# Kernel optimization log

Hardware: AMD Instinct MI355X
Metric: run time of the kernel (lower is better)

Reference implementation:

```python
import jax, jax.numpy as jnp
import numpy as np

M, IN, H, OUT, B = 64, 64, 256, 1, 4096


def setup_inputs() -> dict:
    key = jax.random.key(0)
    ks = jax.random.split(key, 7)
    s1 = 1.0 / np.sqrt(IN)
    s2 = 1.0 / np.sqrt(H)
    return {
        "xs": jax.random.normal(ks[0], (M, B, IN), dtype=jnp.float32),
        "W1": jax.random.uniform(ks[1], (M, IN, H), minval=-s1, maxval=s1, dtype=jnp.float32),
        "b1": jax.random.uniform(ks[2], (M, H), minval=-s1, maxval=s1, dtype=jnp.float32),
        "W2": jax.random.uniform(ks[3], (M, H, H), minval=-s2, maxval=s2, dtype=jnp.float32),
        "b2": jax.random.uniform(ks[4], (M, H), minval=-s2, maxval=s2, dtype=jnp.float32),
        "W3": jax.random.uniform(ks[5], (M, H, OUT), minval=-s2, maxval=s2, dtype=jnp.float32),
        "b3": jax.random.uniform(ks[6], (M, OUT), minval=-s2, maxval=s2, dtype=jnp.float32),
    }


def reference(xs, W1, b1, W2, b2, W3, b3):
    # Batched over models: [M, B, in] x [M, in, h] -> [M, B, h]
    h1 = jax.nn.relu(jnp.einsum("mbi,mih->mbh", xs, W1) + b1[:, None, :])
    h2 = jax.nn.relu(jnp.einsum("mbh,mhk->mbk", h1, W2) + b2[:, None, :])
    out = jnp.einsum("mbh,mho->mbo", h2, W3) + b3[:, None, :]
    return out  # [M, B, out]
```

## Files before the change

### kernel.cpp

```cpp
#include <hip/hip_runtime.h>
#include <hip/hip_bf16.h>

#define NMODELS 64
#define BBATCH  4096
#define IN_DIM  64
#define H_DIM   256

typedef __attribute__((ext_vector_type(8))) short short8;
typedef __attribute__((ext_vector_type(4))) float floatx4;
typedef __attribute__((ext_vector_type(4))) unsigned int uint4v;
typedef __attribute__((ext_vector_type(2))) unsigned int uint2v;

__device__ __forceinline__ unsigned short f2bf(float f) {
    unsigned int u = __builtin_bit_cast(unsigned int, f);
    return (unsigned short)((u + 0x8000u) >> 16);
}
__device__ __forceinline__ unsigned int pkbf(float a, float b) {
    __hip_bfloat162 h = __float22bfloat162_rn(make_float2(a, b));
    unsigned int u;
    __builtin_memcpy(&u, &h, 4);
    return u;
}

__global__ __launch_bounds__(256) void prep_weights(const float* __restrict__ W1,
                                                    const float* __restrict__ W2,
                                                    unsigned short* __restrict__ w1t,
                                                    unsigned short* __restrict__ w2t) {
    __shared__ float lds[64][65];
    const int bid = blockIdx.x;
    const float* src;
    unsigned short* dst;
    int K, N, m, kb, nb;
    if (bid < 256) {
        m = bid >> 2; kb = 0; nb = bid & 3; K = IN_DIM; N = H_DIM;
        src = W1; dst = w1t;
    } else {
        int t = bid - 256;
        m = t >> 4; kb = (t >> 2) & 3; nb = t & 3; K = H_DIM; N = H_DIM;
        src = W2; dst = w2t;
    }
    const float* s = src + ((size_t)m * K + (size_t)kb * 64) * N + nb * 64;
    const int tid = threadIdx.x;
    const int r = tid >> 4, c4 = (tid & 15) * 4;
#pragma unroll
    for (int p = 0; p < 4; ++p) {
        int row = p * 16 + r;
        float4 v = *(const float4*)(s + (size_t)row * N + c4);
        lds[row][c4] = v.x; lds[row][c4 + 1] = v.y;
        lds[row][c4 + 2] = v.z; lds[row][c4 + 3] = v.w;
    }
    __syncthreads();
    unsigned short* dbase = dst + ((size_t)m * N + (size_t)nb * 64) * K + kb * 64;
    const int j = tid & 7;
#pragma unroll
    for (int it = 0; it < 2; ++it) {
        int n = it * 32 + (tid >> 3);
        unsigned short tmp[8];
#pragma unroll
        for (int e = 0; e < 8; ++e) tmp[e] = f2bf(lds[j * 8 + e][n]);
        *(short8*)(dbase + (size_t)n * K + j * 8) = *(const short8*)tmp;
    }
}

__global__ __launch_bounds__(256, 3) void mlp_fused(
    const float* __restrict__ xs,
    const unsigned short* __restrict__ w1t,
    const float* __restrict__ b1,
    const unsigned short* __restrict__ w2t,
    const float* __restrict__ b2,
    const float* __restrict__ w3,
    const float* __restrict__ b3,
    float* __restrict__ out)
{
    __shared__ unsigned short h1s[64 * 256];
    float* red = (float*)&h1s[0];

    const int bid  = blockIdx.x;
    const int m    = bid >> 6;
    const int tile = bid & 63;
    const int tid  = threadIdx.x;
    const int w    = tid >> 6;
    const int lane = tid & 63;
    const int q    = lane >> 4;
    const int c16  = lane & 15;
    const int sw   = c16 & 7;

    floatx4 b1v = *(const floatx4*)(b1 + m * H_DIM + w * 64 + c16 * 4);
    floatx4 b2v = *(const floatx4*)(b2 + m * H_DIM + w * 64 + c16 * 4);
    floatx4 w3v = *(const floatx4*)(w3 + m * H_DIM + w * 64 + c16 * 4);
    const float b3v = b3[m];

    const float* xrow0 = xs + ((size_t)m * BBATCH + (size_t)tile * 64) * IN_DIM;
    const unsigned short* w1p = w1t + (size_t)m * (H_DIM * IN_DIM)
                                + (w * 64 + c16 * 4) * IN_DIM + q * 8;
    const unsigned short* w2p = w2t + (size_t)m * (H_DIM * H_DIM)
                                + (w * 64 + c16 * 4) * H_DIM + q * 8;

    short8 ax[4][2];
#pragma unroll
    for (int rb = 0; rb < 4; ++rb)
#pragma unroll
        for (int kb = 0; kb < 2; ++kb) {
            const float* xp = xrow0 + (rb * 16 + c16) * IN_DIM + kb * 32 + q * 8;
            float4 v0 = *(const float4*)xp;
            float4 v1 = *(const float4*)(xp + 4);
            uint4v u;
            u[0] = pkbf(v0.x, v0.y); u[1] = pkbf(v0.z, v0.w);
            u[2] = pkbf(v1.x, v1.y); u[3] = pkbf(v1.z, v1.w);
            ax[rb][kb] = __builtin_bit_cast(short8, u);
        }

    floatx4 acc[4][4];
#pragma unroll
    for (int rb = 0; rb < 4; ++rb)
#pragma unroll
        for (int nb = 0; nb < 4; ++nb)
            acc[rb][nb] = (floatx4){0.f, 0.f, 0.f, 0.f};

    {
        short8 bw[2][4];
#pragma unroll
        for (int kb = 0; kb < 2; ++kb)
#pragma unroll
            for (int nb = 0; nb < 4; ++nb)
                bw[kb][nb] = *(const short8*)(w1p + nb * IN_DIM + kb * 32);
#pragma unroll
        for (int kb = 0; kb < 2; ++kb)
#pragma unroll
            for (int nb = 0; nb < 4; ++nb)
#pragma unroll
                for (int rb = 0; rb < 4; ++rb)
                    acc[rb][nb] = __builtin_amdgcn_mfma_f32_16x16x32_bf16(
                        ax[rb][kb], bw[kb][nb], acc[rb][nb], 0, 0, 0);
    }

    short8 bv[2][4];
#pragma unroll
    for (int nb = 0; nb < 4; ++nb)
        bv[0][nb] = *(const short8*)(w2p + nb * H_DIM);

    {
#pragma unroll
        for (int rb = 0; rb < 4; ++rb)
#pragma unroll
            for (int r = 0; r < 4; ++r) {
                float v0 = fmaxf(acc[rb][0][r] + b1v[0], 0.f);
                float v1 = fmaxf(acc[rb][1][r] + b1v[1], 0.f);
                float v2 = fmaxf(acc[rb][2][r] + b1v[2], 0.f);
                float v3 = fmaxf(acc[rb][3][r] + b1v[3], 0.f);
                uint2v u2; u2[0] = pkbf(v0, v1); u2[1] = pkbf(v2, v3);
                int row = rb * 16 + q * 4 + r;
                int chunk = (w * 8 + (c16 >> 1)) ^ (row & 7);
                *(uint2v*)((char*)&h1s[0] + row * 512 + chunk * 16 + (c16 & 1) * 8) = u2;
            }
    }
    __syncthreads();

#pragma unroll
    for (int rb = 0; rb < 4; ++rb)
#pragma unroll
        for (int nb = 0; nb < 4; ++nb)
            acc[rb][nb] = (floatx4){0.f, 0.f, 0.f, 0.f};

#pragma unroll
    for (int kb = 0; kb < 8; ++kb) {
        if (kb < 7) {
#pragma unroll
            for (int nb = 0; nb < 4; ++nb)
                bv[(kb + 1) & 1][nb] = *(const short8*)(w2p + nb * H_DIM + (kb + 1) * 32);
        }
        short8 av[4];
#pragma unroll
        for (int rb = 0; rb < 4; ++rb)
            av[rb] = *(const short8*)((char*)&h1s[0] + (rb * 16 + c16) * 512
                                      + (((kb * 4 + q) ^ sw) * 16));
#pragma unroll
        for (int nb = 0; nb < 4; ++nb)
#pragma unroll
            for (int rb = 0; rb < 4; ++rb)
                acc[rb][nb] = __builtin_amdgcn_mfma_f32_16x16x32_bf16(
                    av[rb], bv[kb & 1][nb], acc[rb][nb], 0, 0, 0);
    }

    float p[4][4];
#pragma unroll
    for (int rb = 0; rb < 4; ++rb)
#pragma unroll
        for (int r = 0; r < 4; ++r) p[rb][r] = 0.f;
#pragma unroll
    for (int rb = 0; rb < 4; ++rb)
#pragma unroll
        for (int nb = 0; nb < 4; ++nb)
#pragma unroll
            for (int r = 0; r < 4; ++r) {
                float v = fmaxf(acc[rb][nb][r] + b2v[nb], 0.f);
                p[rb][r] += v * w3v[nb];
            }
#pragma unroll
    for (int off = 1; off < 16; off <<= 1)
#pragma unroll
        for (int rb = 0; rb < 4; ++rb)
#pragma unroll
            for (int r = 0; r < 4; ++r)
                p[rb][r] += __shfl_xor(p[rb][r], off);

    __syncthreads();
    if (c16 == 0) {
#pragma unroll
        for (int rb = 0; rb < 4; ++rb)
#pragma unroll
            for (int r = 0; r < 4; ++r)
                red[w * 64 + rb * 16 + q * 4 + r] = p[rb][r];
    }
    __syncthreads();
    if (tid < 64) {
        float s = red[tid] + red[64 + tid] + red[128 + tid] + red[192 + tid] + b3v;
        out[(size_t)m * BBATCH + tile * 64 + tid] = s;
    }
}

extern "C" void kernel_launch(void* const* d_in, const int* in_sizes, int n_in,
                              void* d_out, int out_size, void* d_ws, size_t ws_size,
                              hipStream_t stream) {
    const float* xs = (const float*)d_in[0];
    const float* W1 = (const float*)d_in[1];
    const float* b1 = (const float*)d_in[2];
    const float* W2 = (const float*)d_in[3];
    const float* b2 = (const float*)d_in[4];
    const float* W3 = (const float*)d_in[5];
    const float* b3 = (const float*)d_in[6];
    float* out = (float*)d_out;

    unsigned short* w1t = (unsigned short*)d_ws;
    unsigned short* w2t = w1t + (size_t)NMODELS * H_DIM * IN_DIM;

    prep_weights<<<256 + NMODELS * 16, 256, 0, stream>>>(W1, W2, w1t, w2t);
    mlp_fused<<<NMODELS * (BBATCH / 64), 256, 0, stream>>>(xs, w1t, b1, w2t, b2, W3, b3, out);
}
```

Before: 215.3 us.

## Give each wave full hidden width over private rows, removing block barriers

Each workgroup now processes 128 batch rows instead of 64. Each wave owns 16 rows of each of two tiles and computes all 256 hidden units, so h1 stays in per-wave LDS and the final reduction needs no cross-wave barrier or LDS step. Block indices are also remapped so that consecutive blocks spread across models, and launch bounds drop to 2 blocks per CU. In exchange, each wave loads the full W2 slice for its model from global memory, with no double-buffered prefetch, and uses many more accumulator registers.

```diff
diff --git a/kernel.cpp b/kernel.cpp
--- a/kernel.cpp
+++ b/kernel.cpp
@@ -62,7 +62,7 @@
     }
 }
 
-__global__ __launch_bounds__(256, 3) void mlp_fused(
+__global__ __launch_bounds__(256, 2) void mlp_fused(
     const float* __restrict__ xs,
     const unsigned short* __restrict__ w1t,
     const float* __restrict__ b1,
@@ -72,12 +72,12 @@
     const float* __restrict__ b3,
     float* __restrict__ out)
 {
-    __shared__ unsigned short h1s[64 * 256];
-    float* red = (float*)&h1s[0];
-
-    const int bid  = blockIdx.x;
-    const int m    = bid >> 6;
-    const int tile = bid & 63;
+    __shared__ unsigned short h1s[2 * 4 * 16 * 256];
+
+    const int bid = blockIdx.x;
+    const int wg  = (bid & 7) * 256 + (bid >> 3);
+    const int m     = wg >> 5;
+    const int tile0 = (wg & 31) * 2;
     const int tid  = threadIdx.x;
     const int w    = tid >> 6;
     const int lane = tid & 63;
@@ -85,137 +85,145 @@
     const int c16  = lane & 15;
     const int sw   = c16 & 7;
 
-    floatx4 b1v = *(const floatx4*)(b1 + m * H_DIM + w * 64 + c16 * 4);
-    floatx4 b2v = *(const floatx4*)(b2 + m * H_DIM + w * 64 + c16 * 4);
-    floatx4 w3v = *(const floatx4*)(w3 + m * H_DIM + w * 64 + c16 * 4);
+    char* const myLds = (char*)h1s + w * 8192;
+
+    floatx4 b1v[4];
+#pragma unroll
+    for (int g = 0; g < 4; ++g)
+        b1v[g] = *(const floatx4*)(b1 + m * H_DIM + g * 64 + c16 * 4);
     const float b3v = b3[m];
 
-    const float* xrow0 = xs + ((size_t)m * BBATCH + (size_t)tile * 64) * IN_DIM;
-    const unsigned short* w1p = w1t + (size_t)m * (H_DIM * IN_DIM)
-                                + (w * 64 + c16 * 4) * IN_DIM + q * 8;
-    const unsigned short* w2p = w2t + (size_t)m * (H_DIM * H_DIM)
-                                + (w * 64 + c16 * 4) * H_DIM + q * 8;
-
-    short8 ax[4][2];
-#pragma unroll
-    for (int rb = 0; rb < 4; ++rb)
+    const float* xrow = xs + ((size_t)m * BBATCH + (size_t)tile0 * 64 + w * 16) * IN_DIM;
+    short8 ax[2][2];
+#pragma unroll
+    for (int t = 0; t < 2; ++t)
 #pragma unroll
         for (int kb = 0; kb < 2; ++kb) {
-            const float* xp = xrow0 + (rb * 16 + c16) * IN_DIM + kb * 32 + q * 8;
+            const float* xp = xrow + (size_t)t * 64 * IN_DIM + c16 * IN_DIM + kb * 32 + q * 8;
             float4 v0 = *(const float4*)xp;
             float4 v1 = *(const float4*)(xp + 4);
             uint4v u;
             u[0] = pkbf(v0.x, v0.y); u[1] = pkbf(v0.z, v0.w);
             u[2] = pkbf(v1.x, v1.y); u[3] = pkbf(v1.z, v1.w);
-            ax[rb][kb] = __builtin_bit_cast(short8, u);
+            ax[t][kb] = __builtin_bit_cast(short8, u);
         }
 
-    floatx4 acc[4][4];
-#pragma unroll
-    for (int rb = 0; rb < 4; ++rb)
-#pragma unroll
-        for (int nb = 0; nb < 4; ++nb)
-            acc[rb][nb] = (floatx4){0.f, 0.f, 0.f, 0.f};
-
-    {
+    floatx4 acc[2][4][4];
+#pragma unroll
+    for (int t = 0; t < 2; ++t)
+#pragma unroll
+        for (int g = 0; g < 4; ++g)
+#pragma unroll
+            for (int nb = 0; nb < 4; ++nb)
+                acc[t][g][nb] = (floatx4){0.f, 0.f, 0.f, 0.f};
+
+    const unsigned short* w1p = w1t + (size_t)m * (H_DIM * IN_DIM)
+                                + (c16 * 4) * IN_DIM + q * 8;
+#pragma unroll
+    for (int g = 0; g < 4; ++g) {
         short8 bw[2][4];
 #pragma unroll
         for (int kb = 0; kb < 2; ++kb)
 #pragma unroll
             for (int nb = 0; nb < 4; ++nb)
-                bw[kb][nb] = *(const short8*)(w1p + nb * IN_DIM + kb * 32);
-#pragma unroll
-        for (int kb = 0; kb < 2; ++kb)
-#pragma unroll
-            for (int nb = 0; nb < 4; ++nb)
-#pragma unroll
-                for (int rb = 0; rb < 4; ++rb)
-                    acc[rb][nb] = __builtin_amdgcn_mfma_f32_16x16x32_bf16(
-                        ax[rb][kb], bw[kb][nb], acc[rb][nb], 0, 0, 0);
-    }
-
-    short8 bv[2][4];
-#pragma unroll
-    for (int nb = 0; nb < 4; ++nb)
-        bv[0][nb] = *(const short8*)(w2p + nb * H_DIM);
-
-    {
-#pragma unroll
-        for (int rb = 0; rb < 4; ++rb)
+                bw[kb][nb] = *(const short8*)(w1p + (size_t)(g * 64 + nb) * IN_DIM + kb * 32);
+#pragma unroll
+        for (int t = 0; t < 2; ++t)
+#pragma unroll
+            for (int kb = 0; kb < 2; ++kb)
+#pragma unroll
+                for (int nb = 0; nb < 4; ++nb)
+                    acc[t][g][nb] = __builtin_amdgcn_mfma_f32_16x16x32_bf16(
+                        ax[t][kb], bw[kb][nb], acc[t][g][nb], 0, 0, 0);
+    }
+
+#pragma unroll
+    for (int t = 0; t < 2; ++t)
+#pragma unroll
+        for (int g = 0; g < 4; ++g)
 #pragma unroll
             for (int r = 0; r < 4; ++r) {
-                float v0 = fmaxf(acc[rb][0][r] + b1v[0], 0.f);
-                float v1 = fmaxf(acc[rb][1][r] + b1v[1], 0.f);
-                float v2 = fmaxf(acc[rb][2][r] + b1v[2], 0.f);
-                float v3 = fmaxf(acc[rb][3][r] + b1v[3], 0.f);
+                float v0 = fmaxf(acc[t][g][0][r] + b1v[g][0], 0.f);
+                float v1 = fmaxf(acc[t][g][1][r] + b1v[g][1], 0.f);
+                float v2 = fmaxf(acc[t][g][2][r] + b1v[g][2], 0.f);
+                float v3 = fmaxf(acc[t][g][3][r] + b1v[g][3], 0.f);
                 uint2v u2; u2[0] = pkbf(v0, v1); u2[1] = pkbf(v2, v3);
-                int row = rb * 16 + q * 4 + r;
-                int chunk = (w * 8 + (c16 >> 1)) ^ (row & 7);
-                *(uint2v*)((char*)&h1s[0] + row * 512 + chunk * 16 + (c16 & 1) * 8) = u2;
+                int row = q * 4 + r;
+                int chunk = (g * 8 + (c16 >> 1)) ^ (row & 7);
+                *(uint2v*)(myLds + t * 32768 + row * 512 + chunk * 16 + (c16 & 1) * 8) = u2;
             }
-    }
-    __syncthreads();
-
-#pragma unroll
-    for (int rb = 0; rb < 4; ++rb)
-#pragma unroll
-        for (int nb = 0; nb < 4; ++nb)
-            acc[rb][nb] = (floatx4){0.f, 0.f, 0.f, 0.f};
-
+
+#pragma unroll
+    for (int t = 0; t < 2; ++t)
+#pragma unroll
+        for (int g = 0; g < 4; ++g)
+#pragma unroll
+            for (int nb = 0; nb < 4; ++nb)
+                acc[t][g][nb] = (floatx4){0.f, 0.f, 0.f, 0.f};
+
+    const unsigned short* w2p = w2t + (size_t)m * (H_DIM * H_DIM)
+                                + (c16 * 4) * H_DIM + q * 8;
 #pragma unroll
     for (int kb = 0; kb < 8; ++kb) {
-        if (kb < 7) {
-#pragma unroll
-            for (int nb = 0; nb < 4; ++nb)
-                bv[(kb + 1) & 1][nb] = *(const short8*)(w2p + nb * H_DIM + (kb + 1) * 32);
+        short8 av[2];
+#pragma unroll
+        for (int t = 0; t < 2; ++t)
+            av[t] = *(const short8*)(myLds + t * 32768 + c16 * 512
+                                     + (((kb * 4 + q) ^ sw) * 16));
+#pragma unroll
+        for (int g = 0; g < 4; ++g) {
+            short8 bv[4];
+#pragma unroll
+            for (int nb = 0; nb < 4; ++nb)
+                bv[nb] = *(const short8*)(w2p + (size_t)(g * 64 + nb) * H_DIM + kb * 32);
+#pragma unroll
+            for (int nb = 0; nb < 4; ++nb)
+#pragma unroll
+                for (int t = 0; t < 2; ++t)
+                    acc[t][g][nb] = __builtin_amdgcn_mfma_f32_16x16x32_bf16(
+                        av[t], bv[nb], acc[t][g][nb], 0, 0, 0);
         }
-        short8 av[4];
-#pragma unroll
-        for (int rb = 0; rb < 4; ++rb)
-            av[rb] = *(const short8*)((char*)&h1s[0] + (rb * 16 + c16) * 512
-                                      + (((kb * 4 + q) ^ sw) * 16));
-#pragma unroll
-        for (int nb = 0; nb < 4; ++nb)
-#pragma unroll
-            for (int rb = 0; rb < 4; ++rb)
-                acc[rb][nb] = __builtin_amdgcn_mfma_f32_16x16x32_bf16(
-                    av[rb], bv[kb & 1][nb], acc[rb][nb], 0, 0, 0);
-    }
-
-    float p[4][4];
-#pragma unroll
-    for (int rb = 0; rb < 4; ++rb)
-#pragma unroll
-        for (int r = 0; r < 4; ++r) p[rb][r] = 0.f;
-#pragma unroll
-    for (int rb = 0; rb < 4; ++rb)
-#pragma unroll
-        for (int nb = 0; nb < 4; ++nb)
-#pragma unroll
-            for (int r = 0; r < 4; ++r) {
-                float v = fmaxf(acc[rb][nb][r] + b2v[nb], 0.f);
-                p[rb][r] += v * w3v[nb];
-            }
+    }
+
+    floatx4 b2v[4], w3v[4];
+#pragma unroll
+    for (int g = 0; g < 4; ++g) {
+        b2v[g] = *(const floatx4*)(b2 + m * H_DIM + g * 64 + c16 * 4);
+        w3v[g] = *(const floatx4*)(w3 + m * H_DIM + g * 64 + c16 * 4);
+    }
+    float pp[2][4];
+#pragma unroll
+    for (int t = 0; t < 2; ++t)
+#pragma unroll
+        for (int r = 0; r < 4; ++r) pp[t][r] = 0.f;
+#pragma unroll
+    for (int t = 0; t < 2; ++t)
+#pragma unroll
+        for (int g = 0; g < 4; ++g)
+#pragma unroll
+            for (int nb = 0; nb < 4; ++nb)
+#pragma unroll
+                for (int r = 0; r < 4; ++r) {
+                    float v = fmaxf(acc[t][g][nb][r] + b2v[g][nb], 0.f);
+                    pp[t][r] += v * w3v[g][nb];
+                }
 #pragma unroll
     for (int off = 1; off < 16; off <<= 1)
 #pragma unroll
-        for (int rb = 0; rb < 4; ++rb)
+        for (int t = 0; t < 2; ++t)
 #pragma unroll
             for (int r = 0; r < 4; ++r)
-                p[rb][r] += __shfl_xor(p[rb][r], off);
-
-    __syncthreads();
+                pp[t][r] += __shfl_xor(pp[t][r], off);
+
     if (c16 == 0) {
 #pragma unroll
-        for (int rb = 0; rb < 4; ++rb)
-#pragma unroll
-            for (int r = 0; r < 4; ++r)
-                red[w * 64 + rb * 16 + q * 4 + r] = p[rb][r];
-    }
-    __syncthreads();
-    if (tid < 64) {
-        float s = red[tid] + red[64 + tid] + red[128 + tid] + red[192 + tid] + b3v;
-        out[(size_t)m * BBATCH + tile * 64 + tid] = s;
+        for (int t = 0; t < 2; ++t) {
+            float4 o;
+            o.x = pp[t][0] + b3v; o.y = pp[t][1] + b3v;
+            o.z = pp[t][2] + b3v; o.w = pp[t][3] + b3v;
+            *(float4*)(out + (size_t)m * BBATCH + (size_t)(tile0 + t) * 64
+                       + w * 16 + q * 4) = o;
+        }
     }
 }
 
@@ -235,5 +243,5 @@
     unsigned short* w2t = w1t + (size_t)NMODELS * H_DIM * IN_DIM;
 
     prep_weights<<<256 + NMODELS * 16, 256, 0, stream>>>(W1, W2, w1t, w2t);
-    mlp_fused<<<NMODELS * (BBATCH / 64), 256, 0, stream>>>(xs, w1t, b1, w2t, b2, W3, b3, out);
-}
+    mlp_fused<<<NMODELS * (BBATCH / 128), 256, 0, stream>>>(xs, w1t, b1, w2t, b2, W3, b3, out);
+}
```

New measurement: 258.3 us. 20.0% more time.

## Process two batch tiles per workgroup with prefetched inputs and XCD-aware block mapping

Applied to the files above, without the earlier changes.

Each workgroup now handles two 64-row tiles in sequence. It prefetches the second tile's x rows into registers while the first tile's epilogue runs, and gives MFMA sections higher wave priority with s_setprio. Block IDs are remapped so consecutive blocks on the same XCD share a model, which improves L2 reuse of that model's weights. The grid is halved and the reduction buffer gets its own LDS, so register pressure and LDS use rise and occupancy may drop.

```diff
diff --git a/kernel.cpp b/kernel.cpp
--- a/kernel.cpp
+++ b/kernel.cpp
@@ -73,73 +73,94 @@
     float* __restrict__ out)
 {
     __shared__ unsigned short h1s[64 * 256];
-    float* red = (float*)&h1s[0];
-
-    const int bid  = blockIdx.x;
-    const int m    = bid >> 6;
-    const int tile = bid & 63;
-    const int tid  = threadIdx.x;
-    const int w    = tid >> 6;
+    __shared__ float red[2 * 256];
+
+    const int bid = blockIdx.x;
+    const int wg  = (bid & 7) * 256 + (bid >> 3);
+    const int m     = wg >> 5;
+    const int tile0 = (wg & 31) * 2;
+    const int tid = threadIdx.x;
+    const int w   = tid >> 6;
     const int lane = tid & 63;
-    const int q    = lane >> 4;
-    const int c16  = lane & 15;
-    const int sw   = c16 & 7;
+    const int q   = lane >> 4;
+    const int c16 = lane & 15;
+    const int sw  = c16 & 7;
 
     floatx4 b1v = *(const floatx4*)(b1 + m * H_DIM + w * 64 + c16 * 4);
-    floatx4 b2v = *(const floatx4*)(b2 + m * H_DIM + w * 64 + c16 * 4);
-    floatx4 w3v = *(const floatx4*)(w3 + m * H_DIM + w * 64 + c16 * 4);
-    const float b3v = b3[m];
-
-    const float* xrow0 = xs + ((size_t)m * BBATCH + (size_t)tile * 64) * IN_DIM;
+
+    const float* xrow0 = xs + ((size_t)m * BBATCH + (size_t)tile0 * 64) * IN_DIM;
     const unsigned short* w1p = w1t + (size_t)m * (H_DIM * IN_DIM)
                                 + (w * 64 + c16 * 4) * IN_DIM + q * 8;
     const unsigned short* w2p = w2t + (size_t)m * (H_DIM * H_DIM)
                                 + (w * 64 + c16 * 4) * H_DIM + q * 8;
 
-    short8 ax[4][2];
-#pragma unroll
-    for (int rb = 0; rb < 4; ++rb)
+    float4 xr[4][2][2];
+    float p[2][4][4];
+    floatx4 b2v, w3v;
+    float b3v;
+
+#pragma unroll
+    for (int t = 0; t < 2; ++t) {
+        short8 ax[4][2];
+        if (t == 0) {
+#pragma unroll
+            for (int rb = 0; rb < 4; ++rb)
+#pragma unroll
+                for (int kb = 0; kb < 2; ++kb) {
+                    const float* xp = xrow0 + (rb * 16 + c16) * IN_DIM + kb * 32 + q * 8;
+                    float4 v0 = *(const float4*)xp;
+                    float4 v1 = *(const float4*)(xp + 4);
+                    uint4v u;
+                    u[0] = pkbf(v0.x, v0.y); u[1] = pkbf(v0.z, v0.w);
+                    u[2] = pkbf(v1.x, v1.y); u[3] = pkbf(v1.z, v1.w);
+                    ax[rb][kb] = __builtin_bit_cast(short8, u);
+                }
+        } else {
+#pragma unroll
+            for (int rb = 0; rb < 4; ++rb)
+#pragma unroll
+                for (int kb = 0; kb < 2; ++kb) {
+                    const float4 v0 = xr[rb][kb][0], v1 = xr[rb][kb][1];
+                    uint4v u;
+                    u[0] = pkbf(v0.x, v0.y); u[1] = pkbf(v0.z, v0.w);
+                    u[2] = pkbf(v1.x, v1.y); u[3] = pkbf(v1.z, v1.w);
+                    ax[rb][kb] = __builtin_bit_cast(short8, u);
+                }
+        }
+
+        floatx4 acc[4][4];
+#pragma unroll
+        for (int rb = 0; rb < 4; ++rb)
+#pragma unroll
+            for (int nb = 0; nb < 4; ++nb)
+                acc[rb][nb] = (floatx4){0.f, 0.f, 0.f, 0.f};
 #pragma unroll
         for (int kb = 0; kb < 2; ++kb) {
-            const float* xp = xrow0 + (rb * 16 + c16) * IN_DIM + kb * 32 + q * 8;
-            float4 v0 = *(const float4*)xp;
-            float4 v1 = *(const float4*)(xp + 4);
-            uint4v u;
-            u[0] = pkbf(v0.x, v0.y); u[1] = pkbf(v0.z, v0.w);
-            u[2] = pkbf(v1.x, v1.y); u[3] = pkbf(v1.z, v1.w);
-            ax[rb][kb] = __builtin_bit_cast(short8, u);
-        }
-
-    floatx4 acc[4][4];
-#pragma unroll
-    for (int rb = 0; rb < 4; ++rb)
-#pragma unroll
-        for (int nb = 0; nb < 4; ++nb)
-            acc[rb][nb] = (floatx4){0.f, 0.f, 0.f, 0.f};
-
-    {
-        short8 bw[2][4];
-#pragma unroll
-        for (int kb = 0; kb < 2; ++kb)
-#pragma unroll
-            for (int nb = 0; nb < 4; ++nb)
-                bw[kb][nb] = *(const short8*)(w1p + nb * IN_DIM + kb * 32);
-#pragma unroll
-        for (int kb = 0; kb < 2; ++kb)
+            short8 bw[4];
+#pragma unroll
+            for (int nb = 0; nb < 4; ++nb)
+                bw[nb] = *(const short8*)(w1p + nb * IN_DIM + kb * 32);
+            __builtin_amdgcn_s_setprio(1);
 #pragma unroll
             for (int nb = 0; nb < 4; ++nb)
 #pragma unroll
                 for (int rb = 0; rb < 4; ++rb)
                     acc[rb][nb] = __builtin_amdgcn_mfma_f32_16x16x32_bf16(
-                        ax[rb][kb], bw[kb][nb], acc[rb][nb], 0, 0, 0);
-    }
-
-    short8 bv[2][4];
-#pragma unroll
-    for (int nb = 0; nb < 4; ++nb)
-        bv[0][nb] = *(const short8*)(w2p + nb * H_DIM);
-
-    {
+                        ax[rb][kb], bw[nb], acc[rb][nb], 0, 0, 0);
+            __builtin_amdgcn_s_setprio(0);
+        }
+
+        short8 bv[2][4];
+#pragma unroll
+        for (int nb = 0; nb < 4; ++nb)
+            bv[0][nb] = *(const short8*)(w2p + nb * H_DIM);
+
+        if (t == 0) {
+            b2v = *(const floatx4*)(b2 + m * H_DIM + w * 64 + c16 * 4);
+            w3v = *(const floatx4*)(w3 + m * H_DIM + w * 64 + c16 * 4);
+            b3v = b3[m];
+        }
+
 #pragma unroll
         for (int rb = 0; rb < 4; ++rb)
 #pragma unroll
@@ -153,69 +174,89 @@
                 int chunk = (w * 8 + (c16 >> 1)) ^ (row & 7);
                 *(uint2v*)((char*)&h1s[0] + row * 512 + chunk * 16 + (c16 & 1) * 8) = u2;
             }
+        __syncthreads();
+
+#pragma unroll
+        for (int rb = 0; rb < 4; ++rb)
+#pragma unroll
+            for (int nb = 0; nb < 4; ++nb)
+                acc[rb][nb] = (floatx4){0.f, 0.f, 0.f, 0.f};
+#pragma unroll
+        for (int kb = 0; kb < 8; ++kb) {
+            if (kb < 7) {
+#pragma unroll
+                for (int nb = 0; nb < 4; ++nb)
+                    bv[(kb + 1) & 1][nb] = *(const short8*)(w2p + nb * H_DIM + (kb + 1) * 32);
+            }
+            short8 av[4];
+#pragma unroll
+            for (int rb = 0; rb < 4; ++rb)
+                av[rb] = *(const short8*)((char*)&h1s[0] + (rb * 16 + c16) * 512
+                                          + (((kb * 4 + q) ^ sw) * 16));
+            __builtin_amdgcn_s_setprio(1);
+#pragma unroll
+            for (int nb = 0; nb < 4; ++nb)
+#pragma unroll
+                for (int rb = 0; rb < 4; ++rb)
+                    acc[rb][nb] = __builtin_amdgcn_mfma_f32_16x16x32_bf16(
+                        av[rb], bv[kb & 1][nb], acc[rb][nb], 0, 0, 0);
+            __builtin_amdgcn_s_setprio(0);
+        }
+
+#pragma unroll
+        for (int rb = 0; rb < 4; ++rb)
+#pragma unroll
+            for (int r = 0; r < 4; ++r) p[t][rb][r] = 0.f;
+#pragma unroll
+        for (int rb = 0; rb < 4; ++rb)
+#pragma unroll
+            for (int nb = 0; nb < 4; ++nb)
+#pragma unroll
+                for (int r = 0; r < 4; ++r) {
+                    float v = fmaxf(acc[rb][nb][r] + b2v[nb], 0.f);
+                    p[t][rb][r] += v * w3v[nb];
+                }
+
+        if (t == 0) {
+            __builtin_amdgcn_sched_barrier(0);
+#pragma unroll
+            for (int rb = 0; rb < 4; ++rb)
+#pragma unroll
+                for (int kb = 0; kb < 2; ++kb) {
+                    const float* xp = xrow0 + 64 * IN_DIM
+                                      + (rb * 16 + c16) * IN_DIM + kb * 32 + q * 8;
+                    xr[rb][kb][0] = *(const float4*)xp;
+                    xr[rb][kb][1] = *(const float4*)(xp + 4);
+                }
+        }
+
+#pragma unroll
+        for (int off = 1; off < 16; off <<= 1)
+#pragma unroll
+            for (int rb = 0; rb < 4; ++rb)
+#pragma unroll
+                for (int r = 0; r < 4; ++r)
+                    p[t][rb][r] += __shfl_xor(p[t][rb][r], off);
+
+        if (t == 0)
+            __syncthreads();
+    }
+
+    if (c16 == 0) {
+#pragma unroll
+        for (int t = 0; t < 2; ++t)
+#pragma unroll
+            for (int rb = 0; rb < 4; ++rb)
+#pragma unroll
+                for (int r = 0; r < 4; ++r)
+                    red[t * 256 + w * 64 + rb * 16 + q * 4 + r] = p[t][rb][r];
     }
     __syncthreads();
-
-#pragma unroll
-    for (int rb = 0; rb < 4; ++rb)
-#pragma unroll
-        for (int nb = 0; nb < 4; ++nb)
-            acc[rb][nb] = (floatx4){0.f, 0.f, 0.f, 0.f};
-
-#pragma unroll
-    for (int kb = 0; kb < 8; ++kb) {
-        if (kb < 7) {
-#pragma unroll
-            for (int nb = 0; nb < 4; ++nb)
-                bv[(kb + 1) & 1][nb] = *(const short8*)(w2p + nb * H_DIM + (kb + 1) * 32);
-        }
-        short8 av[4];
-#pragma unroll
-        for (int rb = 0; rb < 4; ++rb)
-            av[rb] = *(const short8*)((char*)&h1s[0] + (rb * 16 + c16) * 512
-                                      + (((kb * 4 + q) ^ sw) * 16));
-#pragma unroll
-        for (int nb = 0; nb < 4; ++nb)
-#pragma unroll
-            for (int rb = 0; rb < 4; ++rb)
-                acc[rb][nb] = __builtin_amdgcn_mfma_f32_16x16x32_bf16(
-                    av[rb], bv[kb & 1][nb], acc[rb][nb], 0, 0, 0);
-    }
-
-    float p[4][4];
-#pragma unroll
-    for (int rb = 0; rb < 4; ++rb)
-#pragma unroll
-        for (int r = 0; r < 4; ++r) p[rb][r] = 0.f;
-#pragma unroll
-    for (int rb = 0; rb < 4; ++rb)
-#pragma unroll
-        for (int nb = 0; nb < 4; ++nb)
-#pragma unroll
-            for (int r = 0; r < 4; ++r) {
-                float v = fmaxf(acc[rb][nb][r] + b2v[nb], 0.f);
-                p[rb][r] += v * w3v[nb];
-            }
-#pragma unroll
-    for (int off = 1; off < 16; off <<= 1)
-#pragma unroll
-        for (int rb = 0; rb < 4; ++rb)
-#pragma unroll
-            for (int r = 0; r < 4; ++r)
-                p[rb][r] += __shfl_xor(p[rb][r], off);
-
-    __syncthreads();
-    if (c16 == 0) {
-#pragma unroll
-        for (int rb = 0; rb < 4; ++rb)
-#pragma unroll
-            for (int r = 0; r < 4; ++r)
-                red[w * 64 + rb * 16 + q * 4 + r] = p[rb][r];
-    }
-    __syncthreads();
-    if (tid < 64) {
-        float s = red[tid] + red[64 + tid] + red[128 + tid] + red[192 + tid] + b3v;
-        out[(size_t)m * BBATCH + tile * 64 + tid] = s;
+    if (tid < 128) {
+        int t = tid >> 6, rr = tid & 63;
+        const float* rt = red + t * 256;
+        float s = rt[rr] + rt[64 + rr] + rt[128 + rr] + rt[192 + rr] + b3v;
+        out[(size_t)m * BBATCH + (tile0 + t) * 64 + rr] = s;
     }
 }
 
@@ -235,5 +276,5 @@
     unsigned short* w2t = w1t + (size_t)NMODELS * H_DIM * IN_DIM;
 
     prep_weights<<<256 + NMODELS * 16, 256, 0, stream>>>(W1, W2, w1t, w2t);
-    mlp_fused<<<NMODELS * (BBATCH / 64), 256, 0, stream>>>(xs, w1t, b1, w2t, b2, W3, b3, out);
-}
+    mlp_fused<<<NMODELS * (BBATCH / 128), 256, 0, stream>>>(xs, w1t, b1, w2t, b2, W3, b3, out);
+}
```

Result: slower. 222.9 us (+3.5%).
